# Kernel optimization log

Measured on AMD Instinct MI355X. Metric: run time of the kernel, lower is better.

The kernel has to match this reference:

```python
import jax, jax.numpy as jnp
import numpy as np
from math import sqrt

IMG_SIZE = 512
FMAP = IMG_SIZE // 32            # 16
RATIOS = (1.0 / 3.0, 0.5, 1.0, 2.0, 3.0)
SCALE = 0.35
N_CLASSES = 21                   # class 0 = background
MIN_SCORE = 0.01
MAX_OVERLAP = 0.45
BATCH = 16


def make_anchors():
    # mirrors DetectionBaseline.create_anchors (cx, cy, w, h in [0,1])
    anchors = []
    for i in range(FMAP):
        for j in range(FMAP):
            cx = (j + 0.5) / FMAP
            cy = (i + 0.5) / FMAP
            for r in RATIOS:
                anchors.append([cx, cy, SCALE * sqrt(r), SCALE / sqrt(r)])
    return jnp.clip(jnp.asarray(anchors, dtype=jnp.float32), 0.0, 1.0)


def setup_inputs() -> dict:
    key = jax.random.key(0)
    k1, k2 = jax.random.split(key)
    A = FMAP * FMAP * len(RATIOS)  # 1280 anchors
    return {
        "predicted_locs": jax.random.normal(k1, (BATCH, A, 4), dtype=jnp.float32),
        "predicted_scores": jax.random.normal(k2, (BATCH, A, N_CLASSES), dtype=jnp.float32),
        "anchors": make_anchors(),
        "top_k": 200,
    }


def _pairwise_iou(boxes):
    # boxes: [B, A, 4] xyxy -> iou [B, A, A]
    area = (boxes[..., 2] - boxes[..., 0]) * (boxes[..., 3] - boxes[..., 1])
    lt = jnp.maximum(boxes[:, :, None, :2], boxes[:, None, :, :2])
    rb = jnp.minimum(boxes[:, :, None, 2:], boxes[:, None, :, 2:])
    wh = jnp.clip(rb - lt, 0.0, None)
    inter = wh[..., 0] * wh[..., 1]
    union = area[:, :, None] + area[:, None, :] - inter
    return inter / union


def reference(predicted_locs, predicted_scores, anchors, top_k):
    B, A, C = predicted_scores.shape
    Cf = C - 1  # foreground classes
    scores = jax.nn.softmax(predicted_scores, axis=2)  # [B, A, C]

    # standard SSD decode (gcxgcywh -> cxcywh -> xyxy)
    cxcy = predicted_locs[..., :2] * anchors[:, 2:] / 10.0 + anchors[:, :2]
    wh = jnp.exp(predicted_locs[..., 2:] / 5.0) * anchors[:, 2:]
    boxes = jnp.concatenate([cxcy - wh / 2.0, cxcy + wh / 2.0], axis=-1)  # [B, A, 4]

    iou = _pairwise_iou(boxes)  # [B, A, A], shared across classes

    cls_scores = jnp.transpose(scores[:, :, 1:], (0, 2, 1))  # [B, Cf, A]
    valid = cls_scores > MIN_SCORE
    order = jnp.argsort(-cls_scores, axis=-1)  # per-class descending score order

    bi = jnp.arange(B)[:, None]   # [B, 1]
    ci = jnp.arange(Cf)[None, :]  # [1, Cf]

    def step(suppress, idx_r):
        # idx_r: [B, Cf] anchor index processed at this rank
        row = iou[bi, idx_r, :] > MAX_OVERLAP            # [B, Cf, A]
        active = (~suppress[bi, ci, idx_r]) & valid[bi, ci, idx_r]  # [B, Cf]
        new = jnp.where(active[..., None], suppress | row, suppress)
        # original sets suppress[box] = 0 after suppressing its overlaps
        new = new.at[bi, ci, idx_r].set(jnp.where(active, False, new[bi, ci, idx_r]))
        return new, None

    suppress0 = jnp.zeros((B, Cf, A), dtype=bool)
    suppress, _ = jax.lax.scan(step, suppress0, jnp.transpose(order, (2, 0, 1)))
    keep = (~suppress) & valid  # [B, Cf, A]

    # gather top_k detections per image across (class, anchor)
    masked = jnp.where(keep, cls_scores, -1.0).reshape(B, Cf * A)
    topv, topi = jax.lax.top_k(masked, top_k)  # [B, top_k]
    cls_idx = topi // A + 1
    anc_idx = topi % A
    det_valid = topv > 0.0
    out_scores = jnp.where(det_valid, topv, 0.0)
    out_labels = jnp.where(det_valid, cls_idx, 0)
    out_boxes = jnp.where(det_valid[..., None], boxes[bi, anc_idx, :], 0.0)
    return out_boxes, out_labels, out_scores
```

## Files before the change

### kernel.cpp

```cpp
#include <hip/hip_runtime.h>
#include <stdint.h>


#define A_N     1280
#define CF      20
#define NC      21
#define B_N     16
#define TOPK    200
#define THREADS 256
#define CTHREADS 512
#define SORT_N  2048
#define CH      128

#define KEYS_BYTES   (B_N * CF * TOPK * 8)
#define BOX_OFF      KEYS_BYTES
#define MS_OFF       (BOX_OFF + B_N * A_N * 16)
#define WS_B_BYTES   (MS_OFF + B_N * A_N * 8)

static __device__ __forceinline__ uint64_t pack_key(float sc, uint32_t idx) {
    return ((uint64_t)(uint32_t)(~__float_as_uint(sc)) << 32) | (uint64_t)idx;
}

static __device__ __forceinline__ float box_area(const float4 v) {
    return (v.z - v.x) * (v.w - v.y);
}

static __device__ __forceinline__ bool iou_gt(const float4 a, const float aarea,
                                              const float4 b, const float barea) {
    const float lx = fmaxf(a.x, b.x);
    const float ly = fmaxf(a.y, b.y);
    const float rx = fminf(a.z, b.z);
    const float ry = fminf(a.w, b.w);
    const float wx = fmaxf(rx - lx, 0.0f);
    const float wy = fmaxf(ry - ly, 0.0f);
    const float inter = wx * wy;
    const float uni   = aarea + barea - inter;
    return inter / uni > 0.45f;
}

static __device__ __forceinline__ float4 decode_box(const float4 lc, const float4 an) {
    const float cx = lc.x * an.z / 10.0f + an.x;
    const float cy = lc.y * an.w / 10.0f + an.y;
    const float w  = expf(lc.z / 5.0f) * an.z;
    const float h  = expf(lc.w / 5.0f) * an.w;
    float4 v;
    v.x = cx - w / 2.0f; v.y = cy - h / 2.0f;
    v.z = cx + w / 2.0f; v.w = cy + h / 2.0f;
    return v;
}

static __device__ __forceinline__ float4 shfl_box(const float4 v, int lane) {
    float4 r;
    r.x = __shfl(v.x, lane, 64);
    r.y = __shfl(v.y, lane, 64);
    r.z = __shfl(v.z, lane, 64);
    r.w = __shfl(v.w, lane, 64);
    return r;
}

static __device__ __forceinline__ uint64_t readlane_u64(uint64_t v, int lane) {
    const uint32_t lo = (uint32_t)__builtin_amdgcn_readlane((int)(uint32_t)v, lane);
    const uint32_t hi = (uint32_t)__builtin_amdgcn_readlane((int)(uint32_t)(v >> 32), lane);
    return ((uint64_t)hi << 32) | lo;
}

__global__ __launch_bounds__(THREADS)
void prep_kernel(const float* __restrict__ locs,
                 const float* __restrict__ scores,
                 const float* __restrict__ anchors,
                 float4* __restrict__ boxes_ws,
                 float2* __restrict__ ms_ws)
{
    const int g = blockIdx.x * THREADS + threadIdx.x;
    if (g >= B_N * A_N) return;
    const int a = g % A_N;
    boxes_ws[g] = decode_box(((const float4*)locs)[g], ((const float4*)anchors)[a]);
    const float* sp = scores + (size_t)g * NC;
    float m = sp[0];
    #pragma unroll
    for (int k = 1; k < NC; ++k) m = fmaxf(m, sp[k]);
    float sum = 0.0f;
    #pragma unroll
    for (int k = 0; k < NC; ++k) sum += expf(sp[k] - m);
    ms_ws[g] = make_float2(m, sum);
}

__global__ __launch_bounds__(CTHREADS)
void fused_nms_kernel(const float* __restrict__ scores,
                      const float2* __restrict__ ms_ws,
                      const float4* __restrict__ boxes_ws,
                      uint64_t* __restrict__ ws_keys)
{
    __shared__ uint64_t      skeys[SORT_N];
    __shared__ uint64_t      srow[CH][2];
    __shared__ unsigned char sdead[CH];
    __shared__ float4        swbox[TOPK];
    __shared__ float         swarea[TOPK];
    __shared__ uint64_t      swkey[TOPK];
    __shared__ int           sW;

    const int blk = blockIdx.x;
    const int b   = blk / CF;
    const int c   = blk % CF + 1;
    const int t   = threadIdx.x;
    const int l   = t & 63;
    const int w   = t >> 6;

    #pragma unroll
    for (int i = 0; i < SORT_N / CTHREADS; ++i) {
        const int a = t + i * CTHREADS;
        if (a < A_N) {
            const float2 ms = ms_ws[b * A_N + a];
            const float  sl = scores[((size_t)b * A_N + a) * NC + c];
            const float  sc = expf(sl - ms.x) / ms.y;
            skeys[a] = (sc > 0.01f) ? pack_key(sc, (uint32_t)a) : ~0ull;
        } else {
            skeys[a] = ~0ull;
        }
    }
    if (t == 0) sW = 0;
    __syncthreads();

    uint64_t k[4];
    #pragma unroll
    for (int r = 0; r < 4; ++r) k[r] = skeys[(w << 8) + (r << 6) + l];

    for (int kk = 2; kk <= SORT_N; kk <<= 1) {
        for (int j = kk >> 1; j; j >>= 1) {
            if (j >= 256) {
                __syncthreads();
                #pragma unroll
                for (int r = 0; r < 4; ++r) skeys[(w << 8) + (r << 6) + l] = k[r];
                __syncthreads();
                #pragma unroll
                for (int r = 0; r < 4; ++r) {
                    const int e = (w << 8) + (r << 6) + l;
                    const uint64_t o = skeys[e ^ j];
                    const bool keep_min = (((e & j) == 0) == ((e & kk) == 0));
                    const uint64_t mn = k[r] < o ? k[r] : o;
                    const uint64_t mx = k[r] < o ? o : k[r];
                    k[r] = keep_min ? mn : mx;
                }
            } else if (j >= 64) {
                const int rb = j >> 6;
                #pragma unroll
                for (int r = 0; r < 4; ++r) {
                    if ((r & rb) == 0) {
                        const int p = r | rb;
                        const int e = (w << 8) + (r << 6) + l;
                        const bool up = ((e & kk) == 0);
                        const uint64_t x = k[r], y = k[p];
                        const uint64_t mn = x < y ? x : y;
                        const uint64_t mx = x < y ? y : x;
                        k[r] = up ? mn : mx;
                        k[p] = up ? mx : mn;
                    }
                }
            } else {
                #pragma unroll
                for (int r = 0; r < 4; ++r) {
                    const uint64_t o = (uint64_t)__shfl_xor((unsigned long long)k[r], j, 64);
                    const int e = (w << 8) + (r << 6) + l;
                    const bool keep_min = (((e & j) == 0) == ((e & kk) == 0));
                    const uint64_t mn = k[r] < o ? k[r] : o;
                    const uint64_t mx = k[r] < o ? o : k[r];
                    k[r] = keep_min ? mn : mx;
                }
            }
        }
    }
    __syncthreads();
    #pragma unroll
    for (int r = 0; r < 4; ++r) skeys[(w << 8) + (r << 6) + l] = k[r];
    __syncthreads();

    const float4* const bbase = boxes_ws + (size_t)b * A_N;
    int W = 0;
    for (int cb = 0; cb < A_N; cb += CH) {
        if (skeys[cb] == ~0ull) break;

        const uint64_t key0 = skeys[cb + l];
        const uint64_t key1 = skeys[cb + 64 + l];
        const bool v0 = (key0 != ~0ull), v1 = (key1 != ~0ull);
        const float4 box_lo = v0 ? bbase[(uint32_t)key0] : make_float4(-8.f, -8.f, -8.f, -8.f);
        const float4 box_hi = v1 ? bbase[(uint32_t)key1] : make_float4(-8.f, -8.f, -8.f, -8.f);
        const float  al = box_area(box_lo);
        const float  ah = box_area(box_hi);

        {
            const int bx = t >> 2, q = t & 3;
            const uint64_t keyx = skeys[cb + bx];
            const bool valid = (keyx != ~0ull);
            const float4 bv = valid ? bbase[(uint32_t)keyx] : make_float4(-8.f, -8.f, -8.f, -8.f);
            const float  av = box_area(bv);
            int dead = valid ? 0 : 1;
            #pragma unroll 4
            for (int i = q; i < W; i += 4) {
                dead |= iou_gt(swbox[i], swarea[i], bv, av) ? 1 : 0;
            }
            dead |= __shfl_xor(dead, 1, 64);
            dead |= __shfl_xor(dead, 2, 64);
            if (q == 0) sdead[bx] = (unsigned char)dead;
        }
        __syncthreads();

        {
            const int rbase = w * 16;
            uint32_t rm = (uint32_t)__ballot(l < 16 && !sdead[rbase + l]) & 0xFFFFu;
            while (rm) {
                const int j = __ffs(rm) - 1; rm &= rm - 1;
                const int row = rbase + j;
                const float4 rowsrc = (row < 64) ? box_lo : box_hi;
                const float4 rbx = shfl_box(rowsrc, row & 63);
                const float  ra  = box_area(rbx);
                const uint64_t m0 = __ballot(iou_gt(rbx, ra, box_lo, al));
                const uint64_t m1 = __ballot(iou_gt(rbx, ra, box_hi, ah));
                if (l == 0) { srow[row][0] = m0; srow[row][1] = m1; }
            }
        }
        __syncthreads();

        if (w == 0) {
            const uint64_t r0lo = srow[l][0];
            const uint64_t r0hi = srow[l][1];
            const uint64_t r1lo = srow[64 + l][0];
            const uint64_t r1hi = srow[64 + l][1];
            uint64_t alive0 = __ballot(sdead[l] == 0);
            uint64_t alive1 = __ballot(sdead[64 + l] == 0);
            int Wl = W;
            while ((alive0 | alive1) && Wl < TOPK) {
                const int f = alive0 ? __builtin_ctzll(alive0)
                                     : 64 + __builtin_ctzll(alive1);
                if (f < 64) {
                    if (l == f)      { swkey[Wl] = key0; swbox[Wl] = box_lo; swarea[Wl] = al; }
                } else {
                    if (l == f - 64) { swkey[Wl] = key1; swbox[Wl] = box_hi; swarea[Wl] = ah; }
                }
                uint64_t klo, khi;
                if (f < 64) { klo = readlane_u64(r0lo, f);      khi = readlane_u64(r0hi, f); }
                else        { klo = readlane_u64(r1lo, f - 64); khi = readlane_u64(r1hi, f - 64); }
                alive0 &= ~klo;
                alive1 &= ~khi;
                ++Wl;
            }
            if (l == 0) sW = Wl;
        }
        __syncthreads();
        W = sW;
        if (W >= TOPK) break;
    }

    const uint32_t  base = (uint32_t)(c - 1) * A_N;
    uint64_t* const out  = ws_keys + ((size_t)b * CF + (c - 1)) * TOPK;
    for (int k2 = t; k2 < TOPK; k2 += CTHREADS) {
        if (k2 < W) {
            const uint64_t kk2 = swkey[k2];
            out[k2] = (kk2 & 0xFFFFFFFF00000000ull) | (uint64_t)(base + (uint32_t)kk2);
        } else {
            out[k2] = ~0ull;
        }
    }
}

__global__ __launch_bounds__(THREADS)
void nms_mono(const float* __restrict__ locs,
              const float* __restrict__ scores,
              const float* __restrict__ anchors,
              uint64_t* __restrict__ ws_keys)
{
    __shared__ uint64_t      skeys[SORT_N];
    __shared__ float4        sbox[A_N];
    __shared__ float4        schunk[CH];
    __shared__ uint64_t      srow[CH][2];
    __shared__ float4        swbox[TOPK];
    __shared__ uint64_t      swkey[TOPK];
    __shared__ unsigned char sdead[CH];
    __shared__ int           sW;

    const int blk = blockIdx.x;
    const int b   = blk / CF;
    const int c   = blk % CF + 1;
    const int t   = threadIdx.x;
    const int l   = t & 63;
    const int w   = t >> 6;

    #pragma unroll
    for (int i = 0; i < A_N / THREADS; ++i) {
        const int a = t + i * THREADS;
        const float4 v = decode_box(((const float4*)locs)[(size_t)b * A_N + a],
                                    ((const float4*)anchors)[a]);
        const float* sp = scores + ((size_t)b * A_N + a) * NC;
        float m = sp[0];
        #pragma unroll
        for (int kq = 1; kq < NC; ++kq) m = fmaxf(m, sp[kq]);
        float sum = 0.0f;
        #pragma unroll
        for (int kq = 0; kq < NC; ++kq) sum += expf(sp[kq] - m);
        sbox[a] = v;
        const float sc = expf(sp[c] - m) / sum;
        skeys[a] = (sc > 0.01f) ? pack_key(sc, (uint32_t)a) : ~0ull;
    }
    for (int i = A_N + t; i < SORT_N; i += THREADS) skeys[i] = ~0ull;
    if (t == 0) sW = 0;
    __syncthreads();

    uint64_t k[8];
    #pragma unroll
    for (int r = 0; r < 8; ++r) k[r] = skeys[(w << 9) + (r << 6) + l];
    for (int kk = 2; kk <= SORT_N; kk <<= 1) {
        for (int j = kk >> 1; j; j >>= 1) {
            if (j >= 512) {
                __syncthreads();
                #pragma unroll
                for (int r = 0; r < 8; ++r) skeys[(w << 9) + (r << 6) + l] = k[r];
                __syncthreads();
                #pragma unroll
                for (int r = 0; r < 8; ++r) {
                    const int e = (w << 9) + (r << 6) + l;
                    const uint64_t o = skeys[e ^ j];
                    const bool keep_min = (((e & j) == 0) == ((e & kk) == 0));
                    const uint64_t mn = k[r] < o ? k[r] : o;
                    const uint64_t mx = k[r] < o ? o : k[r];
                    k[r] = keep_min ? mn : mx;
                }
            } else if (j >= 64) {
                const int rb = j >> 6;
                #pragma unroll
                for (int r = 0; r < 8; ++r) {
                    if ((r & rb) == 0) {
                        const int p = r | rb;
                        const int e = (w << 9) + (r << 6) + l;
                        const bool up = ((e & kk) == 0);
                        const uint64_t x = k[r], y = k[p];
                        const uint64_t mn = x < y ? x : y;
                        const uint64_t mx = x < y ? y : x;
                        k[r] = up ? mn : mx;
                        k[p] = up ? mx : mn;
                    }
                }
            } else {
                #pragma unroll
                for (int r = 0; r < 8; ++r) {
                    const uint64_t o = (uint64_t)__shfl_xor((unsigned long long)k[r], j, 64);
                    const int e = (w << 9) + (r << 6) + l;
                    const bool keep_min = (((e & j) == 0) == ((e & kk) == 0));
                    const uint64_t mn = k[r] < o ? k[r] : o;
                    const uint64_t mx = k[r] < o ? o : k[r];
                    k[r] = keep_min ? mn : mx;
                }
            }
        }
    }
    __syncthreads();
    #pragma unroll
    for (int r = 0; r < 8; ++r) skeys[(w << 9) + (r << 6) + l] = k[r];
    __syncthreads();

    int W = 0;
    for (int cb = 0; cb < SORT_N; cb += CH) {
        if (skeys[cb] == ~0ull) break;
        if (t < CH) {
            const uint64_t kc = skeys[cb + t];
            const bool v = (kc != ~0ull);
            schunk[t] = v ? sbox[(uint32_t)kc] : make_float4(-8.f, -8.f, -8.f, -8.f);
            sdead[t]  = v ? 0 : 1;
        }
        __syncthreads();
        const float4 cb0 = schunk[l];
        const float4 cb1 = schunk[64 + l];
        const float  ca0 = box_area(cb0);
        const float  ca1 = box_area(cb1);
        for (int r = w * 32; r < w * 32 + 32; ++r) {
            const float4 rbx = schunk[r];
            const float  ra  = box_area(rbx);
            const uint64_t m0 = __ballot(iou_gt(rbx, ra, cb0, ca0));
            const uint64_t m1 = __ballot(iou_gt(rbx, ra, cb1, ca1));
            if (l == 0) { srow[r][0] = m0; srow[r][1] = m1; }
        }
        {
            const int jj = t >> 1, h = t & 1;
            const float4 bj = schunk[jj];
            const float  aj = box_area(bj);
            int sup = 0;
            for (int w2 = h; w2 < W; w2 += 2) {
                const float4 bw = swbox[w2];
                if (iou_gt(bw, box_area(bw), bj, aj)) { sup = 1; break; }
            }
            sup |= __shfl_xor(sup, 1, 64);
            if (h == 0 && sup) sdead[jj] = 1;
        }
        __syncthreads();
        if (t < 64) {
            bool al0 = !sdead[t];
            bool al1 = !sdead[64 + t];
            int Wl = W;
            while (true) {
                const unsigned long long bal0 = __ballot(al0);
                const unsigned long long bal1 = __ballot(al1);
                if (!(bal0 | bal1)) break;
                const int f = bal0 ? (__ffsll(bal0) - 1) : (64 + __ffsll(bal1) - 1);
                if (t == 0) { swkey[Wl] = skeys[cb + f]; swbox[Wl] = schunk[f]; }
                const uint64_t r0 = srow[f][0];
                const uint64_t r1 = srow[f][1];
                al0 = al0 && !((r0 >> t) & 1);
                al1 = al1 && !((r1 >> t) & 1);
                if (++Wl >= TOPK) break;
            }
            if (t == 0) sW = Wl;
        }
        __syncthreads();
        W = sW;
        if (W >= TOPK) break;
    }

    const uint32_t  base = (uint32_t)(c - 1) * A_N;
    uint64_t* const out  = ws_keys + ((size_t)b * CF + (c - 1)) * TOPK;
    for (int kx = t; kx < TOPK; kx += THREADS) {
        if (kx < W) {
            const uint64_t kk2 = swkey[kx];
            out[kx] = (kk2 & 0xFFFFFFFF00000000ull) | (uint64_t)(base + (uint32_t)kk2);
        } else {
            out[kx] = ~0ull;
        }
    }
}

__global__ __launch_bounds__(THREADS)
void merge_kernel(const float* __restrict__ locs,
                  const float* __restrict__ anchors,
                  const uint64_t* __restrict__ ws_keys,
                  float* __restrict__ out)
{
    __shared__ uint64_t Abuf[20][256];
    __shared__ uint64_t Bbuf[10][256];

    const int b = blockIdx.x;
    const int t = threadIdx.x;
    const uint64_t* const in = ws_keys + (size_t)b * CF * TOPK;

    for (int e = t; e < CF * 256; e += THREADS) {
        const int c = e >> 8, i = e & 255;
        Abuf[c][i] = (i < TOPK) ? in[c * TOPK + i] : ~0ull;
    }

    uint64_t (*src)[256] = Abuf;
    uint64_t (*dst)[256] = Bbuf;
    int n = CF;
    while (n > 1) {
        const int  nm    = n >> 1;
        const bool carry = (n & 1) != 0;
        __syncthreads();
        for (int e = t; e < nm * 256; e += THREADS) {
            const int mm = e >> 8, i = e & 255;
            const uint64_t x = src[2 * mm][i];
            const uint64_t y = src[2 * mm + 1][255 - i];
            dst[mm][i] = x < y ? x : y;
        }
        if (carry)
            for (int i = t; i < 256; i += THREADS) dst[nm][i] = src[n - 1][i];
        for (int j = 128; j; j >>= 1) {
            __syncthreads();
            for (int pp = t; pp < nm * 128; pp += THREADS) {
                const int mm = pp >> 7, qq = pp & 127;
                const int i  = ((qq & ~(j - 1)) << 1) | (qq & (j - 1));
                const uint64_t x = dst[mm][i], y = dst[mm][i + j];
                if (y < x) { dst[mm][i] = y; dst[mm][i + j] = x; }
            }
        }
        uint64_t (*tmp)[256] = src; src = dst; dst = tmp;
        n = nm + (carry ? 1 : 0);
    }
    __syncthreads();

    if (t < TOPK) {
        const uint64_t k = src[0][t];
        float* const boxes_out  = out;
        float* const labels_out = out + (size_t)B_N * TOPK * 4;
        float* const scores_out = out + (size_t)B_N * TOPK * 5;
        const size_t s = (size_t)b * TOPK + t;
        if (k == ~0ull) {
            boxes_out[s * 4 + 0] = 0.0f;
            boxes_out[s * 4 + 1] = 0.0f;
            boxes_out[s * 4 + 2] = 0.0f;
            boxes_out[s * 4 + 3] = 0.0f;
            labels_out[s] = 0.0f;
            scores_out[s] = 0.0f;
        } else {
            const uint32_t flat = (uint32_t)k;
            const int cls = flat / A_N;
            const int a   = flat - cls * A_N;
            const float sc = __uint_as_float(~(uint32_t)(k >> 32));
            const float4 v = decode_box(((const float4*)locs)[(size_t)b * A_N + a],
                                        ((const float4*)anchors)[a]);
            boxes_out[s * 4 + 0] = v.x;
            boxes_out[s * 4 + 1] = v.y;
            boxes_out[s * 4 + 2] = v.z;
            boxes_out[s * 4 + 3] = v.w;
            labels_out[s] = (float)(cls + 1);
            scores_out[s] = sc;
        }
    }
}

extern "C" void kernel_launch(void* const* d_in, const int* in_sizes, int n_in,
                              void* d_out, int out_size, void* d_ws, size_t ws_size,
                              hipStream_t stream) {
    const float* locs    = (const float*)d_in[0];
    const float* scores  = (const float*)d_in[1];
    const float* anchors = (const float*)d_in[2];
    uint64_t* ws_keys  = (uint64_t*)d_ws;
    float4*   boxes_ws = (float4*)((char*)d_ws + BOX_OFF);
    float2*   ms_ws    = (float2*)((char*)d_ws + MS_OFF);
    float*    outp     = (float*)d_out;

    if (ws_size >= (size_t)WS_B_BYTES) {
        hipLaunchKernelGGL(prep_kernel, dim3((B_N * A_N + THREADS - 1) / THREADS),
                           dim3(THREADS), 0, stream, locs, scores, anchors, boxes_ws, ms_ws);
        hipLaunchKernelGGL(fused_nms_kernel, dim3(B_N * CF), dim3(CTHREADS), 0, stream,
                           scores, ms_ws, boxes_ws, ws_keys);
    } else {
        hipLaunchKernelGGL(nms_mono, dim3(B_N * CF), dim3(THREADS), 0, stream,
                           locs, scores, anchors, ws_keys);
    }
    hipLaunchKernelGGL(merge_kernel, dim3(B_N), dim3(THREADS), 0, stream,
                       locs, anchors, ws_keys, outp);
}
```

Baseline: 171.1 us.

## Overlap next-chunk IoU mask build with serial greedy scan; sort on four waves

The bitonic sort now runs on only the first four waves, each holding eight keys in registers. The cross-wave shared-memory exchange therefore happens only for strides of 512 and above, which cuts barrier rounds. The chunked NMS loop is software-pipelined: wave 0 runs the serial greedy selection on the current chunk while waves 1-7 build the IoU bitmask rows for the next chunk into a double buffer. The dead-vs-kept pre-check for the next chunk runs after the barrier. In exchange, half the waves sit idle during the sort. Mask rows are now computed for every row, including dead ones, and mask work for chunks never reached after an early exit is wasted.

New measurement: 223.2 us. 30.4% more time.

```diff
diff --git a/kernel.cpp b/kernel.cpp
--- a/kernel.cpp
+++ b/kernel.cpp
@@ -16,6 +16,8 @@
 #define BOX_OFF      KEYS_BYTES
 #define MS_OFF       (BOX_OFF + B_N * A_N * 16)
 #define WS_B_BYTES   (MS_OFF + B_N * A_N * 8)
+
+#define F4INV make_float4(-8.f, -8.f, -8.f, -8.f)
 
 static __device__ __forceinline__ uint64_t pack_key(float sc, uint32_t idx) {
     return ((uint64_t)(uint32_t)(~__float_as_uint(sc)) << 32) | (uint64_t)idx;
@@ -92,7 +94,7 @@
                       uint64_t* __restrict__ ws_keys)
 {
     __shared__ uint64_t      skeys[SORT_N];
-    __shared__ uint64_t      srow[CH][2];
+    __shared__ uint64_t      srowbuf[2][CH][2];
     __shared__ unsigned char sdead[CH];
     __shared__ float4        swbox[TOPK];
     __shared__ float         swarea[TOPK];
@@ -121,110 +123,106 @@
     if (t == 0) sW = 0;
     __syncthreads();
 
-    uint64_t k[4];
-    #pragma unroll
-    for (int r = 0; r < 4; ++r) k[r] = skeys[(w << 8) + (r << 6) + l];
-
+    const bool sorter = (w < 4);
+    uint64_t k[8];
+    if (sorter) {
+        #pragma unroll
+        for (int r = 0; r < 8; ++r) k[r] = skeys[(w << 9) + (r << 6) + l];
+    }
     for (int kk = 2; kk <= SORT_N; kk <<= 1) {
         for (int j = kk >> 1; j; j >>= 1) {
-            if (j >= 256) {
+            if (j >= 512) {
                 __syncthreads();
-                #pragma unroll
-                for (int r = 0; r < 4; ++r) skeys[(w << 8) + (r << 6) + l] = k[r];
+                if (sorter) {
+                    #pragma unroll
+                    for (int r = 0; r < 8; ++r) skeys[(w << 9) + (r << 6) + l] = k[r];
+                }
                 __syncthreads();
-                #pragma unroll
-                for (int r = 0; r < 4; ++r) {
-                    const int e = (w << 8) + (r << 6) + l;
-                    const uint64_t o = skeys[e ^ j];
-                    const bool keep_min = (((e & j) == 0) == ((e & kk) == 0));
-                    const uint64_t mn = k[r] < o ? k[r] : o;
-                    const uint64_t mx = k[r] < o ? o : k[r];
-                    k[r] = keep_min ? mn : mx;
+                if (sorter) {
+                    #pragma unroll
+                    for (int r = 0; r < 8; ++r) {
+                        const int e = (w << 9) + (r << 6) + l;
+                        const uint64_t o = skeys[e ^ j];
+                        const bool keep_min = (((e & j) == 0) == ((e & kk) == 0));
+                        const uint64_t mn = k[r] < o ? k[r] : o;
+                        const uint64_t mx = k[r] < o ? o : k[r];
+                        k[r] = keep_min ? mn : mx;
+                    }
                 }
             } else if (j >= 64) {
-                const int rb = j >> 6;
-                #pragma unroll
-                for (int r = 0; r < 4; ++r) {
-                    if ((r & rb) == 0) {
-                        const int p = r | rb;
-                        const int e = (w << 8) + (r << 6) + l;
-                        const bool up = ((e & kk) == 0);
-                        const uint64_t x = k[r], y = k[p];
-                        const uint64_t mn = x < y ? x : y;
-                        const uint64_t mx = x < y ? y : x;
-                        k[r] = up ? mn : mx;
-                        k[p] = up ? mx : mn;
+                if (sorter) {
+                    const int rb = j >> 6;
+                    #pragma unroll
+                    for (int r = 0; r < 8; ++r) {
+                        if ((r & rb) == 0) {
+                            const int p = r | rb;
+                            const int e = (w << 9) + (r << 6) + l;
+                            const bool up = ((e & kk) == 0);
+                            const uint64_t x = k[r], y = k[p];
+                            const uint64_t mn = x < y ? x : y;
+                            const uint64_t mx = x < y ? y : x;
+                            k[r] = up ? mn : mx;
+                            k[p] = up ? mx : mn;
+                        }
                     }
                 }
             } else {
-                #pragma unroll
-                for (int r = 0; r < 4; ++r) {
-                    const uint64_t o = (uint64_t)__shfl_xor((unsigned long long)k[r], j, 64);
-                    const int e = (w << 8) + (r << 6) + l;
-                    const bool keep_min = (((e & j) == 0) == ((e & kk) == 0));
-                    const uint64_t mn = k[r] < o ? k[r] : o;
-                    const uint64_t mx = k[r] < o ? o : k[r];
-                    k[r] = keep_min ? mn : mx;
-                }
-            }
-        }
-    }
-    __syncthreads();
-    #pragma unroll
-    for (int r = 0; r < 4; ++r) skeys[(w << 8) + (r << 6) + l] = k[r];
+                if (sorter) {
+                    #pragma unroll
+                    for (int r = 0; r < 8; ++r) {
+                        const uint64_t o = (uint64_t)__shfl_xor((unsigned long long)k[r], j, 64);
+                        const int e = (w << 9) + (r << 6) + l;
+                        const bool keep_min = (((e & j) == 0) == ((e & kk) == 0));
+                        const uint64_t mn = k[r] < o ? k[r] : o;
+                        const uint64_t mx = k[r] < o ? o : k[r];
+                        k[r] = keep_min ? mn : mx;
+                    }
+                }
+            }
+        }
+    }
+    __syncthreads();
+    if (sorter) {
+        #pragma unroll
+        for (int r = 0; r < 8; ++r) skeys[(w << 9) + (r << 6) + l] = k[r];
+    }
     __syncthreads();
 
     const float4* const bbase = boxes_ws + (size_t)b * A_N;
-    int W = 0;
+    {
+        const uint64_t k0 = skeys[l];
+        const uint64_t k1 = skeys[64 + l];
+        const float4 b_lo = (k0 != ~0ull) ? bbase[(uint32_t)k0] : F4INV;
+        const float4 b_hi = (k1 != ~0ull) ? bbase[(uint32_t)k1] : F4INV;
+        const float a_lo = box_area(b_lo), a_hi = box_area(b_hi);
+        const int rb0 = w * 16;
+        for (int row = rb0; row < rb0 + 16; ++row) {
+            const float4 rbx = shfl_box(row < 64 ? b_lo : b_hi, row & 63);
+            const float  ra  = box_area(rbx);
+            const uint64_t m0 = __ballot(iou_gt(rbx, ra, b_lo, a_lo));
+            const uint64_t m1 = __ballot(iou_gt(rbx, ra, b_hi, a_hi));
+            if (l == 0) { srowbuf[0][row][0] = m0; srowbuf[0][row][1] = m1; }
+        }
+    }
+    for (int i = t; i < CH; i += CTHREADS) sdead[i] = (skeys[i] == ~0ull) ? 1 : 0;
+    __syncthreads();
+
+    int W = 0, cur = 0;
     for (int cb = 0; cb < A_N; cb += CH) {
         if (skeys[cb] == ~0ull) break;
 
-        const uint64_t key0 = skeys[cb + l];
-        const uint64_t key1 = skeys[cb + 64 + l];
-        const bool v0 = (key0 != ~0ull), v1 = (key1 != ~0ull);
-        const float4 box_lo = v0 ? bbase[(uint32_t)key0] : make_float4(-8.f, -8.f, -8.f, -8.f);
-        const float4 box_hi = v1 ? bbase[(uint32_t)key1] : make_float4(-8.f, -8.f, -8.f, -8.f);
-        const float  al = box_area(box_lo);
-        const float  ah = box_area(box_hi);
-
-        {
-            const int bx = t >> 2, q = t & 3;
-            const uint64_t keyx = skeys[cb + bx];
-            const bool valid = (keyx != ~0ull);
-            const float4 bv = valid ? bbase[(uint32_t)keyx] : make_float4(-8.f, -8.f, -8.f, -8.f);
-            const float  av = box_area(bv);
-            int dead = valid ? 0 : 1;
-            #pragma unroll 4
-            for (int i = q; i < W; i += 4) {
-                dead |= iou_gt(swbox[i], swarea[i], bv, av) ? 1 : 0;
-            }
-            dead |= __shfl_xor(dead, 1, 64);
-            dead |= __shfl_xor(dead, 2, 64);
-            if (q == 0) sdead[bx] = (unsigned char)dead;
-        }
-        __syncthreads();
-
-        {
-            const int rbase = w * 16;
-            uint32_t rm = (uint32_t)__ballot(l < 16 && !sdead[rbase + l]) & 0xFFFFu;
-            while (rm) {
-                const int j = __ffs(rm) - 1; rm &= rm - 1;
-                const int row = rbase + j;
-                const float4 rowsrc = (row < 64) ? box_lo : box_hi;
-                const float4 rbx = shfl_box(rowsrc, row & 63);
-                const float  ra  = box_area(rbx);
-                const uint64_t m0 = __ballot(iou_gt(rbx, ra, box_lo, al));
-                const uint64_t m1 = __ballot(iou_gt(rbx, ra, box_hi, ah));
-                if (l == 0) { srow[row][0] = m0; srow[row][1] = m1; }
-            }
-        }
-        __syncthreads();
-
         if (w == 0) {
-            const uint64_t r0lo = srow[l][0];
-            const uint64_t r0hi = srow[l][1];
-            const uint64_t r1lo = srow[64 + l][0];
-            const uint64_t r1hi = srow[64 + l][1];
+            const uint64_t key0 = skeys[cb + l];
+            const uint64_t key1 = skeys[cb + 64 + l];
+            const bool v0 = (key0 != ~0ull), v1 = (key1 != ~0ull);
+            const float4 box_lo = v0 ? bbase[(uint32_t)key0] : F4INV;
+            const float4 box_hi = v1 ? bbase[(uint32_t)key1] : F4INV;
+            const float  al = box_area(box_lo);
+            const float  ah = box_area(box_hi);
+            const uint64_t r0lo = srowbuf[cur][l][0];
+            const uint64_t r0hi = srowbuf[cur][l][1];
+            const uint64_t r1lo = srowbuf[cur][64 + l][0];
+            const uint64_t r1hi = srowbuf[cur][64 + l][1];
             uint64_t alive0 = __ballot(sdead[l] == 0);
             uint64_t alive1 = __ballot(sdead[64 + l] == 0);
             int Wl = W;
@@ -244,10 +242,45 @@
                 ++Wl;
             }
             if (l == 0) sW = Wl;
+        } else if (cb + CH < A_N) {
+            const int cbn = cb + CH;
+            const uint64_t nk0 = skeys[cbn + l];
+            const uint64_t nk1 = skeys[cbn + 64 + l];
+            const float4 nb_lo = (nk0 != ~0ull) ? bbase[(uint32_t)nk0] : F4INV;
+            const float4 nb_hi = (nk1 != ~0ull) ? bbase[(uint32_t)nk1] : F4INV;
+            const float  nal = box_area(nb_lo), nah = box_area(nb_hi);
+            const int rb0 = (w - 1) * 19;
+            const int rb1 = (rb0 + 19 < CH) ? rb0 + 19 : CH;
+            for (int row = rb0; row < rb1; ++row) {
+                const float4 rbx = shfl_box(row < 64 ? nb_lo : nb_hi, row & 63);
+                const float  ra  = box_area(rbx);
+                const uint64_t m0 = __ballot(iou_gt(rbx, ra, nb_lo, nal));
+                const uint64_t m1 = __ballot(iou_gt(rbx, ra, nb_hi, nah));
+                if (l == 0) { srowbuf[cur ^ 1][row][0] = m0; srowbuf[cur ^ 1][row][1] = m1; }
+            }
         }
         __syncthreads();
         W = sW;
         if (W >= TOPK) break;
+
+        if (cb + CH < A_N) {
+            const int cbn = cb + CH;
+            const int bx = t >> 2, q = t & 3;
+            const uint64_t keyx = skeys[cbn + bx];
+            const bool valid = (keyx != ~0ull);
+            const float4 bv = valid ? bbase[(uint32_t)keyx] : F4INV;
+            const float  av = box_area(bv);
+            int dead = valid ? 0 : 1;
+            #pragma unroll 4
+            for (int i = q; i < W; i += 4) {
+                dead |= iou_gt(swbox[i], swarea[i], bv, av) ? 1 : 0;
+            }
+            dead |= __shfl_xor(dead, 1, 64);
+            dead |= __shfl_xor(dead, 2, 64);
+            if (q == 0) sdead[bx] = (unsigned char)dead;
+        }
+        __syncthreads();
+        cur ^= 1;
     }
 
     const uint32_t  base = (uint32_t)(c - 1) * A_N;
@@ -362,7 +395,7 @@
         if (t < CH) {
             const uint64_t kc = skeys[cb + t];
             const bool v = (kc != ~0ull);
-            schunk[t] = v ? sbox[(uint32_t)kc] : make_float4(-8.f, -8.f, -8.f, -8.f);
+            schunk[t] = v ? sbox[(uint32_t)kc] : F4INV;
             sdead[t]  = v ? 0 : 1;
         }
         __syncthreads();
```
